# Kernel optimization log

Hardware: AMD Instinct MI355X
Metric: run time of the kernel (lower is better)

The kernel has to match this reference:

```python
import jax, jax.numpy as jnp
import numpy as np

B, N, H, OUT, T = 8192, 82, 10, 5, 3  # batch, n_nodes, hidden, output_channel, time_step


def setup_inputs() -> dict:
    key = jax.random.key(0)
    ks = jax.random.split(key, 20)

    def lin(kw, kb, fin, fout):
        w = jax.random.normal(kw, (fout, fin), jnp.float32) * (1.0 / np.sqrt(fin))
        b = jax.random.normal(kb, (fout,), jnp.float32) * 0.01
        return w, b

    w3w, b3w = lin(ks[0], ks[1], 2 * H, H)
    w3u, b3u = lin(ks[2], ks[3], H, H)
    w4w, b4w = lin(ks[4], ks[5], 2 * H, H)
    w5w, b5w = lin(ks[6], ks[7], 2 * H, H)
    w5u, b5u = lin(ks[8], ks[9], H, H)
    wout, bout = lin(ks[10], ks[11], 2 * H, OUT)
    return {
        'x': jax.random.normal(ks[12], (B, N, H), jnp.float32),
        'in_adj': jax.random.uniform(ks[13], (N, N), jnp.float32),
        'out_adj': jax.random.uniform(ks[14], (N, N), jnp.float32),
        'w3w': w3w, 'b3w': b3w, 'w3u': w3u, 'b3u': b3u,
        'w4w': w4w, 'b4w': b4w, 'w5w': w5w, 'b5w': b5w,
        'w5u': w5u, 'b5u': b5u, 'wout': wout, 'bout': bout,
    }


def _dense(v, w, b):
    return v @ w.T + b


def reference(x, in_adj, out_adj, w3w, b3w, w3u, b3u, w4w, b4w,
              w5w, b5w, w5u, b5u, wout, bout):
    b, n, h = x.shape
    nodes = x  # [B, N, H]
    fn = nodes.reshape(b * n, h)
    for _ in range(T):
        # neighbor aggregation; adjacency shared across batch (torch tiles it with repeat)
        a_in = jnp.einsum('ij,bjh->bih', in_adj, nodes)
        a_out = jnp.einsum('ij,bjh->bih', out_adj, nodes)
        av = jnp.concatenate([a_in, a_out], axis=-1).reshape(b * n, 2 * h)
        fn = nodes.reshape(b * n, h)
        zv = jax.nn.sigmoid(_dense(av, w3w, b3w) + _dense(fn, w3u, b3u))
        # NOTE: original torch code (bug) reuses fc_eq3_u here instead of fc_eq4_u
        rv = jax.nn.sigmoid(_dense(av, w4w, b4w) + _dense(fn, w3u, b3u))
        hv = jnp.tanh(_dense(av, w5w, b5w) + _dense(rv * fn, w5u, b5u))
        fn = (1.0 - zv) * fn + zv * hv
        nodes = fn.reshape(b, n, h)
    out_in = jnp.concatenate([fn, x.reshape(b * n, h)], axis=1)
    output = jnp.tanh(_dense(out_in, wout, bout))
    return output, fn
```

## Files before the change

kernel.cpp:

```cpp
#include <hip/hip_runtime.h>
#include <hip/hip_bf16.h>
#include <math.h>

#define B_TOTAL 8192
#define NN      82
#define HH      10
#define OUTC    5
#define TSTEP   3
#define NB      3
#define THREADS 256
#define KP      96
#define MP      16
#define XS      104
#define UTS     248

typedef __bf16 bf16x8 __attribute__((ext_vector_type(8)));
typedef float  f32x4  __attribute__((ext_vector_type(4)));
typedef float  f32x2  __attribute__((ext_vector_type(2)));

__device__ __forceinline__ float sigmoid_(float x) {
    return 1.0f / (1.0f + __expf(-x));
}
__device__ __forceinline__ float tanh_(float x) {
    float e = __expf(2.0f * x);
    return 1.0f - 2.0f / (e + 1.0f);
}
__device__ __forceinline__ f32x2 ld2(const float* p) {
    return *reinterpret_cast<const f32x2*>(p);
}
__device__ __forceinline__ f32x2 fma2(f32x2 a, f32x2 b, f32x2 c) {
    return __builtin_elementwise_fma(a, b, c);
}

__global__ void prep_adj_kernel(const float* __restrict__ in_adj,
                                const float* __restrict__ out_adj,
                                __hip_bfloat16* __restrict__ adjP) {
    int idx = blockIdx.x * blockDim.x + threadIdx.x;
    if (idx < 2 * KP * KP) {
        int a   = idx / (KP * KP);
        int rem = idx - a * (KP * KP);
        int i = rem / KP;
        int j = rem - i * KP;
        float v = 0.0f;
        if (i < NN && j < NN) v = (a == 0) ? in_adj[i * NN + j] : out_adj[i * NN + j];
        __hip_bfloat16 hi = __float2bfloat16(v);
        __hip_bfloat16 lo = __float2bfloat16(v - __bfloat162float(hi));
        adjP[idx]               = hi;
        adjP[2 * KP * KP + idx] = lo;
    }
}

extern "C" __global__ __launch_bounds__(THREADS, 4)
void ggnn_kernel(const float* __restrict__ x,
                 const __hip_bfloat16* __restrict__ adjP,
                 const float* __restrict__ w3w, const float* __restrict__ b3w,
                 const float* __restrict__ w3u, const float* __restrict__ b3u,
                 const float* __restrict__ w4w, const float* __restrict__ b4w,
                 const float* __restrict__ w5w, const float* __restrict__ b5w,
                 const float* __restrict__ w5u, const float* __restrict__ b5u,
                 const float* __restrict__ wout, const float* __restrict__ bout,
                 float* __restrict__ out0, float* __restrict__ out_fn)
{
    __shared__ __align__(16) __hip_bfloat16 XtH[NB * MP][XS];
    __shared__ __align__(16) __hip_bfloat16 XtL[NB * MP][XS];
    __shared__ float uinT [HH][UTS];
    __shared__ float uoutT[HH][UTS];

    const int t     = threadIdx.x;
    const int bbase = blockIdx.x * NB;
    const int bl    = t / NN;
    const int node  = t - bl * NN;
    const bool act  = (bl < NB) && (bbase + bl < B_TOTAL);
    const int b     = bbase + bl;

    const int lane = t & 63;
    const int w    = t >> 6;
    const int lo16 = lane & 15;
    const int quad = lane >> 4;

    bf16x8 Bh[3][3], Bl[3][3];
    int ntile_c[3], adj_c[3];
    #pragma unroll
    for (int c = 0; c < 3; ++c) {
        int co = w * 3 + c;
        int nt = co >> 1;
        int ad = co & 1;
        ntile_c[c] = nt;
        adj_c[c]   = ad;
        const __hip_bfloat16* BpH = adjP + ((size_t)ad * KP * KP
                                            + (size_t)(nt * 16 + lo16) * KP
                                            + quad * 8);
        #pragma unroll
        for (int k = 0; k < 3; ++k) {
            Bh[c][k] = *reinterpret_cast<const bf16x8*>(BpH + k * 32);
            Bl[c][k] = *reinterpret_cast<const bf16x8*>(BpH + 2 * KP * KP + k * 32);
        }
    }

    for (int idx = t; idx < NB * NN * HH; idx += THREADS) {
        int b_l = idx / (NN * HH);
        int rem = idx - b_l * (NN * HH);
        int j   = rem / HH;
        int h   = rem - j * HH;
        size_t g = (size_t)bbase * NN * HH + idx;
        float v = (g < (size_t)B_TOTAL * NN * HH) ? x[g] : 0.0f;
        __hip_bfloat16 hi = __float2bfloat16(v);
        __hip_bfloat16 lo = __float2bfloat16(v - __bfloat162float(hi));
        XtH[b_l * MP + h][j] = hi;
        XtL[b_l * MP + h][j] = lo;
    }
    for (int idx = t; idx < NB * MP * (KP - NN); idx += THREADS) {
        int r = idx / (KP - NN);
        int c = idx - r * (KP - NN);
        __hip_bfloat16 z = __float2bfloat16(0.0f);
        XtH[r][NN + c] = z;
        XtL[r][NN + c] = z;
    }

    f32x2 fn2[5];
    if (act) {
        const float* xr = x + ((size_t)b * NN + node) * HH;
        #pragma unroll
        for (int p = 0; p < 5; ++p) {
            float2 v = reinterpret_cast<const float2*>(xr)[p];
            fn2[p].x = v.x; fn2[p].y = v.y;
        }
    }

    for (int step = 0; step < TSTEP; ++step) {
        __syncthreads();

        #pragma unroll
        for (int mtile = 0; mtile < NB; ++mtile) {
            f32x4 acc[3] = {{0,0,0,0}, {0,0,0,0}, {0,0,0,0}};
            #pragma unroll
            for (int k = 0; k < 3; ++k) {
                bf16x8 ah = *reinterpret_cast<const bf16x8*>(&XtH[mtile * MP + lo16][quad * 8 + k * 32]);
                bf16x8 al = *reinterpret_cast<const bf16x8*>(&XtL[mtile * MP + lo16][quad * 8 + k * 32]);
                #pragma unroll
                for (int c = 0; c < 3; ++c) {
                    acc[c] = __builtin_amdgcn_mfma_f32_16x16x32_bf16(ah, Bh[c][k], acc[c], 0, 0, 0);
                    acc[c] = __builtin_amdgcn_mfma_f32_16x16x32_bf16(al, Bh[c][k], acc[c], 0, 0, 0);
                    acc[c] = __builtin_amdgcn_mfma_f32_16x16x32_bf16(ah, Bl[c][k], acc[c], 0, 0, 0);
                }
            }
            #pragma unroll
            for (int c = 0; c < 3; ++c) {
                int i = ntile_c[c] * 16 + lo16;
                if (i < NN) {
                    int col = mtile * NN + i;
                    float* plane0 = adj_c[c] ? &uoutT[0][0] : &uinT[0][0];
                    if (quad < 2) {
                        #pragma unroll
                        for (int r = 0; r < 4; ++r)
                            plane0[(quad * 4 + r) * UTS + col] = acc[c][r];
                    } else if (quad == 2) {
                        plane0[8 * UTS + col] = acc[c][0];
                        plane0[9 * UTS + col] = acc[c][1];
                    }
                }
            }
        }

        __syncthreads();

        if (act) {
            f32x2 av2[10];
            #pragma unroll
            for (int p = 0; p < 5; ++p) {
                av2[p].x     = uinT [2 * p][t];
                av2[p].y     = uinT [2 * p + 1][t];
                av2[5 + p].x = uoutT[2 * p][t];
                av2[5 + p].y = uoutT[2 * p + 1][t];
            }

            float u3[HH];
            #pragma unroll
            for (int h = 0; h < HH; ++h) {
                f32x2 s2 = {0.0f, 0.0f};
                #pragma unroll
                for (int p = 0; p < 5; ++p)
                    s2 = fma2(ld2(w3u + h * HH + 2 * p), fn2[p], s2);
                u3[h] = b3u[h] + s2.x + s2.y;
            }

            float zv[HH];
            f32x2 rf2[5];
            #pragma unroll
            for (int h = 0; h < HH; ++h) {
                f32x2 z2 = {0.0f, 0.0f}, r2 = {0.0f, 0.0f};
                #pragma unroll
                for (int p = 0; p < 10; ++p) {
                    z2 = fma2(ld2(w3w + h * 20 + 2 * p), av2[p], z2);
                    r2 = fma2(ld2(w4w + h * 20 + 2 * p), av2[p], r2);
                }
                zv[h] = sigmoid_(b3w[h] + z2.x + z2.y + u3[h]);
                float rv = sigmoid_(b4w[h] + r2.x + r2.y + u3[h]);
                float fnh = (h & 1) ? fn2[h >> 1].y : fn2[h >> 1].x;
                if (h & 1) rf2[h >> 1].y = rv * fnh; else rf2[h >> 1].x = rv * fnh;
            }

            #pragma unroll
            for (int h = 0; h < HH; ++h) {
                f32x2 s2 = {0.0f, 0.0f};
                #pragma unroll
                for (int p = 0; p < 10; ++p)
                    s2 = fma2(ld2(w5w + h * 20 + 2 * p), av2[p], s2);
                #pragma unroll
                for (int p = 0; p < 5; ++p)
                    s2 = fma2(ld2(w5u + h * HH + 2 * p), rf2[p], s2);
                float hv = tanh_(b5w[h] + b5u[h] + s2.x + s2.y);
                float fnh = (h & 1) ? fn2[h >> 1].y : fn2[h >> 1].x;
                fnh = fnh + zv[h] * (hv - fnh);
                if (h & 1) fn2[h >> 1].y = fnh; else fn2[h >> 1].x = fnh;
            }

            #pragma unroll
            for (int h = 0; h < HH; ++h) {
                float fnh = (h & 1) ? fn2[h >> 1].y : fn2[h >> 1].x;
                __hip_bfloat16 hi = __float2bfloat16(fnh);
                __hip_bfloat16 lo = __float2bfloat16(fnh - __bfloat162float(hi));
                XtH[bl * MP + h][node] = hi;
                XtL[bl * MP + h][node] = lo;
            }
        }
    }

    if (act) {
        size_t row = (size_t)b * NN + node;
        const float* xr = x + row * HH;
        f32x2 xi2[5];
        #pragma unroll
        for (int p = 0; p < 5; ++p) {
            float2 v = reinterpret_cast<const float2*>(xr)[p];
            xi2[p].x = v.x; xi2[p].y = v.y;
        }

        #pragma unroll
        for (int c = 0; c < OUTC; ++c) {
            f32x2 s2 = {0.0f, 0.0f};
            #pragma unroll
            for (int p = 0; p < 5; ++p) {
                s2 = fma2(ld2(wout + c * 20 + 2 * p),      fn2[p], s2);
                s2 = fma2(ld2(wout + c * 20 + 10 + 2 * p), xi2[p], s2);
            }
            out0[row * OUTC + c] = tanh_(bout[c] + s2.x + s2.y);
        }
        #pragma unroll
        for (int p = 0; p < 5; ++p) {
            reinterpret_cast<float2*>(out_fn + row * HH)[p] =
                make_float2(fn2[p].x, fn2[p].y);
        }
    }
}

extern "C" void kernel_launch(void* const* d_in, const int* in_sizes, int n_in,
                              void* d_out, int out_size, void* d_ws, size_t ws_size,
                              hipStream_t stream) {
    const float* x       = (const float*)d_in[0];
    const float* in_adj  = (const float*)d_in[1];
    const float* out_adj = (const float*)d_in[2];
    const float* w3w = (const float*)d_in[3];
    const float* b3w = (const float*)d_in[4];
    const float* w3u = (const float*)d_in[5];
    const float* b3u = (const float*)d_in[6];
    const float* w4w = (const float*)d_in[7];
    const float* b4w = (const float*)d_in[8];
    const float* w5w = (const float*)d_in[9];
    const float* b5w = (const float*)d_in[10];
    const float* w5u = (const float*)d_in[11];
    const float* b5u = (const float*)d_in[12];
    const float* wout = (const float*)d_in[13];
    const float* bout = (const float*)d_in[14];

    __hip_bfloat16* adjP = (__hip_bfloat16*)d_ws;
    float* out0   = (float*)d_out;
    float* out_fn = out0 + (size_t)B_TOTAL * NN * OUTC;

    prep_adj_kernel<<<(2 * KP * KP + 255) / 256, 256, 0, stream>>>(in_adj, out_adj, adjP);

    int grid = (B_TOTAL + NB - 1) / NB;
    ggnn_kernel<<<grid, THREADS, 0, stream>>>(
        x, adjP, w3w, b3w, w3u, b3u, w4w, b4w, w5w, b5w, w5u, b5u,
        wout, bout, out0, out_fn);
}
```

Measured before the change: 226.5 us.

## Stage GRU weights and biases in shared memory instead of global loads

Copies all dense-layer weights and biases into a shared-memory array at kernel start and reads them from LDS in the per-node GRU update and output projection, instead of reading them from global or scalar memory. It also lowers the launch-bounds occupancy hint from 4 to 3 blocks per SM and keeps the timestep loop rolled. These are meant to cut global/scalar load traffic and register pressure. The cost is extra LDS use, LDS bank traffic in the inner loops, and possibly lower occupancy.

```diff
diff --git a/kernel.cpp b/kernel.cpp
--- a/kernel.cpp
+++ b/kernel.cpp
@@ -13,6 +13,20 @@
 #define MP      16
 #define XS      104
 #define UTS     248
+
+#define W3W 0
+#define W4W 200
+#define W5W 400
+#define W3U 600
+#define W5U 700
+#define WOUT 800
+#define B3W 900
+#define B4W 910
+#define B5W 920
+#define B3U 930
+#define B5U 940
+#define BOUT 950
+#define WTOT 960
 
 typedef __bf16 bf16x8 __attribute__((ext_vector_type(8)));
 typedef float  f32x4  __attribute__((ext_vector_type(4)));
@@ -50,7 +64,7 @@
     }
 }
 
-extern "C" __global__ __launch_bounds__(THREADS, 4)
+extern "C" __global__ __launch_bounds__(THREADS, 3)
 void ggnn_kernel(const float* __restrict__ x,
                  const __hip_bfloat16* __restrict__ adjP,
                  const float* __restrict__ w3w, const float* __restrict__ b3w,
@@ -65,6 +79,7 @@
     __shared__ __align__(16) __hip_bfloat16 XtL[NB * MP][XS];
     __shared__ float uinT [HH][UTS];
     __shared__ float uoutT[HH][UTS];
+    __shared__ __align__(16) float wS[WTOT];
 
     const int t     = threadIdx.x;
     const int bbase = blockIdx.x * NB;
@@ -77,6 +92,25 @@
     const int w    = t >> 6;
     const int lo16 = lane & 15;
     const int quad = lane >> 4;
+
+    for (int i = t; i < 200; i += THREADS) {
+        wS[W3W + i] = w3w[i];
+        wS[W4W + i] = w4w[i];
+        wS[W5W + i] = w5w[i];
+    }
+    if (t < 100) {
+        wS[W3U + t]  = w3u[t];
+        wS[W5U + t]  = w5u[t];
+        wS[WOUT + t] = wout[t];
+    }
+    if (t < 10) {
+        wS[B3W + t] = b3w[t];
+        wS[B4W + t] = b4w[t];
+        wS[B5W + t] = b5w[t];
+        wS[B3U + t] = b3u[t];
+        wS[B5U + t] = b5u[t];
+    }
+    if (t < OUTC) wS[BOUT + t] = bout[t];
 
     bf16x8 Bh[3][3], Bl[3][3];
     int ntile_c[3], adj_c[3];
@@ -127,6 +161,7 @@
         }
     }
 
+    #pragma unroll 1
     for (int step = 0; step < TSTEP; ++step) {
         __syncthreads();
 
@@ -180,8 +215,8 @@
                 f32x2 s2 = {0.0f, 0.0f};
                 #pragma unroll
                 for (int p = 0; p < 5; ++p)
-                    s2 = fma2(ld2(w3u + h * HH + 2 * p), fn2[p], s2);
-                u3[h] = b3u[h] + s2.x + s2.y;
+                    s2 = fma2(ld2(&wS[W3U + h * HH + 2 * p]), fn2[p], s2);
+                u3[h] = wS[B3U + h] + s2.x + s2.y;
             }
 
             float zv[HH];
@@ -191,11 +226,11 @@
                 f32x2 z2 = {0.0f, 0.0f}, r2 = {0.0f, 0.0f};
                 #pragma unroll
                 for (int p = 0; p < 10; ++p) {
-                    z2 = fma2(ld2(w3w + h * 20 + 2 * p), av2[p], z2);
-                    r2 = fma2(ld2(w4w + h * 20 + 2 * p), av2[p], r2);
+                    z2 = fma2(ld2(&wS[W3W + h * 20 + 2 * p]), av2[p], z2);
+                    r2 = fma2(ld2(&wS[W4W + h * 20 + 2 * p]), av2[p], r2);
                 }
-                zv[h] = sigmoid_(b3w[h] + z2.x + z2.y + u3[h]);
-                float rv = sigmoid_(b4w[h] + r2.x + r2.y + u3[h]);
+                zv[h] = sigmoid_(wS[B3W + h] + z2.x + z2.y + u3[h]);
+                float rv = sigmoid_(wS[B4W + h] + r2.x + r2.y + u3[h]);
                 float fnh = (h & 1) ? fn2[h >> 1].y : fn2[h >> 1].x;
                 if (h & 1) rf2[h >> 1].y = rv * fnh; else rf2[h >> 1].x = rv * fnh;
             }
@@ -205,11 +240,11 @@
                 f32x2 s2 = {0.0f, 0.0f};
                 #pragma unroll
                 for (int p = 0; p < 10; ++p)
-                    s2 = fma2(ld2(w5w + h * 20 + 2 * p), av2[p], s2);
+                    s2 = fma2(ld2(&wS[W5W + h * 20 + 2 * p]), av2[p], s2);
                 #pragma unroll
                 for (int p = 0; p < 5; ++p)
-                    s2 = fma2(ld2(w5u + h * HH + 2 * p), rf2[p], s2);
-                float hv = tanh_(b5w[h] + b5u[h] + s2.x + s2.y);
+                    s2 = fma2(ld2(&wS[W5U + h * HH + 2 * p]), rf2[p], s2);
+                float hv = tanh_(wS[B5W + h] + wS[B5U + h] + s2.x + s2.y);
                 float fnh = (h & 1) ? fn2[h >> 1].y : fn2[h >> 1].x;
                 fnh = fnh + zv[h] * (hv - fnh);
                 if (h & 1) fn2[h >> 1].y = fnh; else fn2[h >> 1].x = fnh;
@@ -241,10 +276,10 @@
             f32x2 s2 = {0.0f, 0.0f};
             #pragma unroll
             for (int p = 0; p < 5; ++p) {
-                s2 = fma2(ld2(wout + c * 20 + 2 * p),      fn2[p], s2);
-                s2 = fma2(ld2(wout + c * 20 + 10 + 2 * p), xi2[p], s2);
-            }
-            out0[row * OUTC + c] = tanh_(bout[c] + s2.x + s2.y);
+                s2 = fma2(ld2(&wS[WOUT + c * 20 + 2 * p]),      fn2[p], s2);
+                s2 = fma2(ld2(&wS[WOUT + c * 20 + 10 + 2 * p]), xi2[p], s2);
+            }
+            out0[row * OUTC + c] = tanh_(wS[BOUT + c] + s2.x + s2.y);
         }
         #pragma unroll
         for (int p = 0; p < 5; ++p) {
```

Result: slower. 264.6 us (+16.8%).

## Move GRU gate dense layers onto MFMA with unified fp32 activation smem

Applied to the files above, without the earlier changes.

Replaces the per-thread scalar FMA gate computations (z, r, h dense layers) with bf16 hi/lo split MFMA tiles that use shared-memory-staged packed weights, with the biases folded in through a constant-one row. Activations now live in one fp32 shared buffer with a swizzled row layout and are converted to bf16 hi/lo on the fly. Adjacency fragments are reloaded from global memory instead of being held in registers. The batch per block drops from 3 to 2 and the occupancy hint rises to 5. This trades extra conversions, extra barriers and global reloads for fewer scalar FMAs and lower register pressure.

```diff
diff --git a/kernel.cpp b/kernel.cpp
--- a/kernel.cpp
+++ b/kernel.cpp
@@ -7,29 +7,27 @@
 #define HH      10
 #define OUTC    5
 #define TSTEP   3
-#define NB      3
+#define NB      2
 #define THREADS 256
 #define KP      96
-#define MP      16
-#define XS      104
-#define UTS     248
+#define CP      204
+#define ACT_FLOATS (32 * CP)
+#define WS_F    6528
+#define GS_F    6640
+#define SMEM_FLOATS 8176
 
 typedef __bf16 bf16x8 __attribute__((ext_vector_type(8)));
 typedef float  f32x4  __attribute__((ext_vector_type(4)));
-typedef float  f32x2  __attribute__((ext_vector_type(2)));
-
+
+__device__ __forceinline__ int aidx(int r, int c) {
+    return r * CP + ((r & 3) << 2) + c;
+}
 __device__ __forceinline__ float sigmoid_(float x) {
     return 1.0f / (1.0f + __expf(-x));
 }
 __device__ __forceinline__ float tanh_(float x) {
     float e = __expf(2.0f * x);
     return 1.0f - 2.0f / (e + 1.0f);
-}
-__device__ __forceinline__ f32x2 ld2(const float* p) {
-    return *reinterpret_cast<const f32x2*>(p);
-}
-__device__ __forceinline__ f32x2 fma2(f32x2 a, f32x2 b, f32x2 c) {
-    return __builtin_elementwise_fma(a, b, c);
 }
 
 __global__ void prep_adj_kernel(const float* __restrict__ in_adj,
@@ -50,7 +48,7 @@
     }
 }
 
-extern "C" __global__ __launch_bounds__(THREADS, 4)
+extern "C" __global__ __launch_bounds__(THREADS, 5)
 void ggnn_kernel(const float* __restrict__ x,
                  const __hip_bfloat16* __restrict__ adjP,
                  const float* __restrict__ w3w, const float* __restrict__ b3w,
@@ -61,25 +59,19 @@
                  const float* __restrict__ wout, const float* __restrict__ bout,
                  float* __restrict__ out0, float* __restrict__ out_fn)
 {
-    __shared__ __align__(16) __hip_bfloat16 XtH[NB * MP][XS];
-    __shared__ __align__(16) __hip_bfloat16 XtL[NB * MP][XS];
-    __shared__ float uinT [HH][UTS];
-    __shared__ float uoutT[HH][UTS];
+    __shared__ __align__(16) float smemF[SMEM_FLOATS];
+    float* actF = smemF;
+    float* wS   = smemF + WS_F;
+    __hip_bfloat16* gS = reinterpret_cast<__hip_bfloat16*>(smemF + GS_F);
 
     const int t     = threadIdx.x;
     const int bbase = blockIdx.x * NB;
-    const int bl    = t / NN;
-    const int node  = t - bl * NN;
-    const bool act  = (bl < NB) && (bbase + bl < B_TOTAL);
-    const int b     = bbase + bl;
-
-    const int lane = t & 63;
-    const int w    = t >> 6;
-    const int lo16 = lane & 15;
-    const int quad = lane >> 4;
-
-    bf16x8 Bh[3][3], Bl[3][3];
-    int ntile_c[3], adj_c[3];
+    const int lane  = t & 63;
+    const int w     = t >> 6;
+    const int lo16  = lane & 15;
+    const int quad  = lane >> 4;
+
+    int ntile_c[3], adj_c[3], Boff[3];
     #pragma unroll
     for (int c = 0; c < 3; ++c) {
         int co = w * 3 + c;
@@ -87,170 +79,196 @@
         int ad = co & 1;
         ntile_c[c] = nt;
         adj_c[c]   = ad;
-        const __hip_bfloat16* BpH = adjP + ((size_t)ad * KP * KP
-                                            + (size_t)(nt * 16 + lo16) * KP
-                                            + quad * 8);
-        #pragma unroll
-        for (int k = 0; k < 3; ++k) {
-            Bh[c][k] = *reinterpret_cast<const bf16x8*>(BpH + k * 32);
-            Bl[c][k] = *reinterpret_cast<const bf16x8*>(BpH + 2 * KP * KP + k * 32);
-        }
-    }
-
+        Boff[c] = ad * KP * KP + (nt * 16 + lo16) * KP + quad * 8;
+    }
+    const int arow = 20 + ((lo16 < 12) ? lo16 : 11);
+
+    for (int i = t; i < ACT_FLOATS; i += THREADS) actF[i] = 0.0f;
+    if (t < 100) wS[t] = wout[t];
+    if (t < OUTC) wS[100 + t] = bout[t];
+    for (int e2 = t; e2 < 3072; e2 += THREADS) {
+        int g   = e2 / 1024;
+        int rem = e2 - g * 1024;
+        int hl  = rem >> 9;
+        int e   = rem & 511;
+        int row = e >> 5;
+        int kc  = e & 31;
+        const float* wW = (g == 0) ? w3w : (g == 1) ? w4w : w5w;
+        const float* wU = (g == 2) ? w5u : w3u;
+        const float* bW = (g == 0) ? b3w : (g == 1) ? b4w : b5w;
+        const float* bU = (g == 2) ? b5u : b3u;
+        float v = 0.0f;
+        if (row < HH) {
+            if (kc < 20)       v = wW[row * 20 + kc];
+            else if (kc < 30)  v = wU[row * 10 + (kc - 20)];
+            else if (kc == 30) v = bW[row] + bU[row];
+        }
+        __hip_bfloat16 hi = __float2bfloat16(v);
+        __hip_bfloat16 lo = __float2bfloat16(v - __bfloat162float(hi));
+        gS[(g * 2 + hl) * 512 + e] = hl ? lo : hi;
+    }
+    __syncthreads();
+    if (t < 192) actF[aidx(30, t)] = 1.0f;
     for (int idx = t; idx < NB * NN * HH; idx += THREADS) {
         int b_l = idx / (NN * HH);
         int rem = idx - b_l * (NN * HH);
         int j   = rem / HH;
         int h   = rem - j * HH;
-        size_t g = (size_t)bbase * NN * HH + idx;
-        float v = (g < (size_t)B_TOTAL * NN * HH) ? x[g] : 0.0f;
-        __hip_bfloat16 hi = __float2bfloat16(v);
-        __hip_bfloat16 lo = __float2bfloat16(v - __bfloat162float(hi));
-        XtH[b_l * MP + h][j] = hi;
-        XtL[b_l * MP + h][j] = lo;
-    }
-    for (int idx = t; idx < NB * MP * (KP - NN); idx += THREADS) {
-        int r = idx / (KP - NN);
-        int c = idx - r * (KP - NN);
-        __hip_bfloat16 z = __float2bfloat16(0.0f);
-        XtH[r][NN + c] = z;
-        XtL[r][NN + c] = z;
-    }
-
-    f32x2 fn2[5];
-    if (act) {
-        const float* xr = x + ((size_t)b * NN + node) * HH;
+        actF[aidx(20 + h, b_l * 96 + j)] = x[(size_t)bbase * NN * HH + idx];
+    }
+
+    #pragma unroll 1
+    for (int step = 0; step < TSTEP; ++step) {
+        __syncthreads();
+
+        f32x4 acc[NB][3];
+        #pragma unroll
+        for (int m = 0; m < NB; ++m)
+            #pragma unroll
+            for (int c = 0; c < 3; ++c) acc[m][c] = (f32x4){0, 0, 0, 0};
+
+        #pragma unroll 1
+        for (int k = 0; k < 3; ++k) {
+            #pragma unroll
+            for (int m = 0; m < NB; ++m) {
+                const float* ap = actF + aidx(arow, m * 96 + quad * 8 + k * 32);
+                f32x4 a0 = *reinterpret_cast<const f32x4*>(ap);
+                f32x4 a1 = *reinterpret_cast<const f32x4*>(ap + 4);
+                bf16x8 ah, al;
+                #pragma unroll
+                for (int e = 0; e < 4; ++e) {
+                    __bf16 h0 = (__bf16)a0[e];
+                    __bf16 h1 = (__bf16)a1[e];
+                    ah[e]     = h0;
+                    ah[4 + e] = h1;
+                    al[e]     = (__bf16)(a0[e] - (float)h0);
+                    al[4 + e] = (__bf16)(a1[e] - (float)h1);
+                }
+                #pragma unroll
+                for (int c = 0; c < 3; ++c) {
+                    const __hip_bfloat16* bp = adjP + Boff[c] + k * 32;
+                    bf16x8 bh = *reinterpret_cast<const bf16x8*>(bp);
+                    bf16x8 bl = *reinterpret_cast<const bf16x8*>(bp + 2 * KP * KP);
+                    acc[m][c] = __builtin_amdgcn_mfma_f32_16x16x32_bf16(ah, bh, acc[m][c], 0, 0, 0);
+                    acc[m][c] = __builtin_amdgcn_mfma_f32_16x16x32_bf16(al, bh, acc[m][c], 0, 0, 0);
+                    acc[m][c] = __builtin_amdgcn_mfma_f32_16x16x32_bf16(ah, bl, acc[m][c], 0, 0, 0);
+                }
+            }
+        }
+        #pragma unroll
+        for (int m = 0; m < NB; ++m) {
+            #pragma unroll
+            for (int c = 0; c < 3; ++c) {
+                int ccol  = m * 96 + ntile_c[c] * 16 + lo16;
+                int rbase = adj_c[c] * 10;
+                if (quad < 2) {
+                    #pragma unroll
+                    for (int r = 0; r < 4; ++r)
+                        actF[aidx(rbase + quad * 4 + r, ccol)] = acc[m][c][r];
+                } else if (quad == 2) {
+                    actF[aidx(rbase + 8, ccol)] = acc[m][c][0];
+                    actF[aidx(rbase + 9, ccol)] = acc[m][c][1];
+                }
+            }
+        }
+
+        __syncthreads();
+
+        #pragma unroll 1
+        for (int tt = 0; tt < 3; ++tt) {
+            const int col  = 48 * w + 16 * tt + lo16;
+            const int cmod = (col >= 96) ? (col - 96) : col;
+            const bool colv = (cmod < NN);
+
+            bf16x8 bh, bl;
+            #pragma unroll
+            for (int jj = 0; jj < 8; ++jj) {
+                float v = actF[aidx(quad * 8 + jj, col)];
+                __bf16 h_ = (__bf16)v;
+                bh[jj] = h_;
+                bl[jj] = (__bf16)(v - (float)h_);
+            }
+            f32x4 az = {0, 0, 0, 0}, ar = {0, 0, 0, 0};
+            {
+                bf16x8 WH = *reinterpret_cast<const bf16x8*>(&gS[0 * 512 + lo16 * 32 + quad * 8]);
+                bf16x8 WL = *reinterpret_cast<const bf16x8*>(&gS[1 * 512 + lo16 * 32 + quad * 8]);
+                az = __builtin_amdgcn_mfma_f32_16x16x32_bf16(WH, bh, az, 0, 0, 0);
+                az = __builtin_amdgcn_mfma_f32_16x16x32_bf16(WL, bh, az, 0, 0, 0);
+                az = __builtin_amdgcn_mfma_f32_16x16x32_bf16(WH, bl, az, 0, 0, 0);
+            }
+            {
+                bf16x8 WH = *reinterpret_cast<const bf16x8*>(&gS[2 * 512 + lo16 * 32 + quad * 8]);
+                bf16x8 WL = *reinterpret_cast<const bf16x8*>(&gS[3 * 512 + lo16 * 32 + quad * 8]);
+                ar = __builtin_amdgcn_mfma_f32_16x16x32_bf16(WH, bh, ar, 0, 0, 0);
+                ar = __builtin_amdgcn_mfma_f32_16x16x32_bf16(WL, bh, ar, 0, 0, 0);
+                ar = __builtin_amdgcn_mfma_f32_16x16x32_bf16(WH, bl, ar, 0, 0, 0);
+            }
+            float zs[4], fc[4];
+            #pragma unroll
+            for (int r = 0; r < 4; ++r) {
+                int h = quad * 4 + r;
+                if (h < HH) {
+                    zs[r] = sigmoid_(az[r]);
+                    fc[r] = actF[aidx(20 + h, col)];
+                    actF[aidx(20 + h, col)] = sigmoid_(ar[r]) * fc[r];
+                }
+            }
+
+            __syncthreads();
+
+            #pragma unroll
+            for (int jj = 0; jj < 8; ++jj) {
+                float v = actF[aidx(quad * 8 + jj, col)];
+                __bf16 h_ = (__bf16)v;
+                bh[jj] = h_;
+                bl[jj] = (__bf16)(v - (float)h_);
+            }
+            f32x4 ah_ = {0, 0, 0, 0};
+            {
+                bf16x8 WH = *reinterpret_cast<const bf16x8*>(&gS[4 * 512 + lo16 * 32 + quad * 8]);
+                bf16x8 WL = *reinterpret_cast<const bf16x8*>(&gS[5 * 512 + lo16 * 32 + quad * 8]);
+                ah_ = __builtin_amdgcn_mfma_f32_16x16x32_bf16(WH, bh, ah_, 0, 0, 0);
+                ah_ = __builtin_amdgcn_mfma_f32_16x16x32_bf16(WL, bh, ah_, 0, 0, 0);
+                ah_ = __builtin_amdgcn_mfma_f32_16x16x32_bf16(WH, bl, ah_, 0, 0, 0);
+            }
+            #pragma unroll
+            for (int r = 0; r < 4; ++r) {
+                int h = quad * 4 + r;
+                if (h < HH && colv) {
+                    float hv = tanh_(ah_[r]);
+                    actF[aidx(20 + h, col)] = fc[r] + zs[r] * (hv - fc[r]);
+                }
+            }
+        }
+    }
+
+    __syncthreads();
+
+    if (t < NB * 96 && (t % 96) < NN) {
+        int m = t / 96, node = t - m * 96;
+        size_t row = (size_t)(bbase + m) * NN + node;
+        float fnv[HH];
+        #pragma unroll
+        for (int h = 0; h < HH; ++h) fnv[h] = actF[aidx(20 + h, t)];
+        const float* xr = x + row * HH;
+        float xi[HH];
         #pragma unroll
         for (int p = 0; p < 5; ++p) {
             float2 v = reinterpret_cast<const float2*>(xr)[p];
-            fn2[p].x = v.x; fn2[p].y = v.y;
-        }
-    }
-
-    for (int step = 0; step < TSTEP; ++step) {
-        __syncthreads();
-
-        #pragma unroll
-        for (int mtile = 0; mtile < NB; ++mtile) {
-            f32x4 acc[3] = {{0,0,0,0}, {0,0,0,0}, {0,0,0,0}};
-            #pragma unroll
-            for (int k = 0; k < 3; ++k) {
-                bf16x8 ah = *reinterpret_cast<const bf16x8*>(&XtH[mtile * MP + lo16][quad * 8 + k * 32]);
-                bf16x8 al = *reinterpret_cast<const bf16x8*>(&XtL[mtile * MP + lo16][quad * 8 + k * 32]);
-                #pragma unroll
-                for (int c = 0; c < 3; ++c) {
-                    acc[c] = __builtin_amdgcn_mfma_f32_16x16x32_bf16(ah, Bh[c][k], acc[c], 0, 0, 0);
-                    acc[c] = __builtin_amdgcn_mfma_f32_16x16x32_bf16(al, Bh[c][k], acc[c], 0, 0, 0);
-                    acc[c] = __builtin_amdgcn_mfma_f32_16x16x32_bf16(ah, Bl[c][k], acc[c], 0, 0, 0);
-                }
-            }
-            #pragma unroll
-            for (int c = 0; c < 3; ++c) {
-                int i = ntile_c[c] * 16 + lo16;
-                if (i < NN) {
-                    int col = mtile * NN + i;
-                    float* plane0 = adj_c[c] ? &uoutT[0][0] : &uinT[0][0];
-                    if (quad < 2) {
-                        #pragma unroll
-                        for (int r = 0; r < 4; ++r)
-                            plane0[(quad * 4 + r) * UTS + col] = acc[c][r];
-                    } else if (quad == 2) {
-                        plane0[8 * UTS + col] = acc[c][0];
-                        plane0[9 * UTS + col] = acc[c][1];
-                    }
-                }
-            }
-        }
-
-        __syncthreads();
-
-        if (act) {
-            f32x2 av2[10];
-            #pragma unroll
-            for (int p = 0; p < 5; ++p) {
-                av2[p].x     = uinT [2 * p][t];
-                av2[p].y     = uinT [2 * p + 1][t];
-                av2[5 + p].x = uoutT[2 * p][t];
-                av2[5 + p].y = uoutT[2 * p + 1][t];
-            }
-
-            float u3[HH];
-            #pragma unroll
-            for (int h = 0; h < HH; ++h) {
-                f32x2 s2 = {0.0f, 0.0f};
-                #pragma unroll
-                for (int p = 0; p < 5; ++p)
-                    s2 = fma2(ld2(w3u + h * HH + 2 * p), fn2[p], s2);
-                u3[h] = b3u[h] + s2.x + s2.y;
-            }
-
-            float zv[HH];
-            f32x2 rf2[5];
-            #pragma unroll
-            for (int h = 0; h < HH; ++h) {
-                f32x2 z2 = {0.0f, 0.0f}, r2 = {0.0f, 0.0f};
-                #pragma unroll
-                for (int p = 0; p < 10; ++p) {
-                    z2 = fma2(ld2(w3w + h * 20 + 2 * p), av2[p], z2);
-                    r2 = fma2(ld2(w4w + h * 20 + 2 * p), av2[p], r2);
-                }
-                zv[h] = sigmoid_(b3w[h] + z2.x + z2.y + u3[h]);
-                float rv = sigmoid_(b4w[h] + r2.x + r2.y + u3[h]);
-                float fnh = (h & 1) ? fn2[h >> 1].y : fn2[h >> 1].x;
-                if (h & 1) rf2[h >> 1].y = rv * fnh; else rf2[h >> 1].x = rv * fnh;
-            }
-
-            #pragma unroll
-            for (int h = 0; h < HH; ++h) {
-                f32x2 s2 = {0.0f, 0.0f};
-                #pragma unroll
-                for (int p = 0; p < 10; ++p)
-                    s2 = fma2(ld2(w5w + h * 20 + 2 * p), av2[p], s2);
-                #pragma unroll
-                for (int p = 0; p < 5; ++p)
-                    s2 = fma2(ld2(w5u + h * HH + 2 * p), rf2[p], s2);
-                float hv = tanh_(b5w[h] + b5u[h] + s2.x + s2.y);
-                float fnh = (h & 1) ? fn2[h >> 1].y : fn2[h >> 1].x;
-                fnh = fnh + zv[h] * (hv - fnh);
-                if (h & 1) fn2[h >> 1].y = fnh; else fn2[h >> 1].x = fnh;
-            }
-
-            #pragma unroll
-            for (int h = 0; h < HH; ++h) {
-                float fnh = (h & 1) ? fn2[h >> 1].y : fn2[h >> 1].x;
-                __hip_bfloat16 hi = __float2bfloat16(fnh);
-                __hip_bfloat16 lo = __float2bfloat16(fnh - __bfloat162float(hi));
-                XtH[bl * MP + h][node] = hi;
-                XtL[bl * MP + h][node] = lo;
-            }
-        }
-    }
-
-    if (act) {
-        size_t row = (size_t)b * NN + node;
-        const float* xr = x + row * HH;
-        f32x2 xi2[5];
-        #pragma unroll
-        for (int p = 0; p < 5; ++p) {
-            float2 v = reinterpret_cast<const float2*>(xr)[p];
-            xi2[p].x = v.x; xi2[p].y = v.y;
-        }
-
+            xi[2 * p] = v.x; xi[2 * p + 1] = v.y;
+        }
         #pragma unroll
         for (int c = 0; c < OUTC; ++c) {
-            f32x2 s2 = {0.0f, 0.0f};
-            #pragma unroll
-            for (int p = 0; p < 5; ++p) {
-                s2 = fma2(ld2(wout + c * 20 + 2 * p),      fn2[p], s2);
-                s2 = fma2(ld2(wout + c * 20 + 10 + 2 * p), xi2[p], s2);
-            }
-            out0[row * OUTC + c] = tanh_(bout[c] + s2.x + s2.y);
-        }
-        #pragma unroll
-        for (int p = 0; p < 5; ++p) {
+            float s = wS[100 + c];
+            #pragma unroll
+            for (int p = 0; p < HH; ++p)
+                s += wS[c * 20 + p] * fnv[p] + wS[c * 20 + 10 + p] * xi[p];
+            out0[row * OUTC + c] = tanh_(s);
+        }
+        #pragma unroll
+        for (int p = 0; p < 5; ++p)
             reinterpret_cast<float2*>(out_fn + row * HH)[p] =
-                make_float2(fn2[p].x, fn2[p].y);
-        }
+                make_float2(fnv[2 * p], fnv[2 * p + 1]);
     }
 }
 
```

Result: slower. 280.5 us (+23.8%).
